# Kernel optimization log

Measured on AMD Instinct MI355X. Metric: run time of the kernel, lower is better.

## Reference

```python
import jax, jax.numpy as jnp
import numpy as np

B, T, H, W, D = 64, 512, 768, 256, 256  # batch, tokens, bert hidden, max words, embedding_dim


def setup_inputs() -> dict:
    key = jax.random.key(0)
    k1, k2, k3 = jax.random.split(key, 3)
    hidden_states = jax.random.normal(k1, (B, T, H), dtype=jnp.float32)
    # word_ids from a fast tokenizer are nondecreasing within a sentence
    word_ids = jnp.sort(jax.random.randint(k2, (B, T), 0, W), axis=-1)
    proj_w = jax.random.normal(k3, (H, D), dtype=jnp.float32) / np.sqrt(H).astype(np.float32)
    proj_b = jnp.zeros((D,), dtype=jnp.float32)
    return {"hidden_states": hidden_states, "word_ids": word_ids,
            "proj_w": proj_w, "proj_b": proj_b}


def _segment_mean(h, wid):
    # h: [T, H], wid: [T]. Invalid ids (<0 or >=W, i.e. special/pad tokens)
    # are routed to a dump segment W that is sliced away.
    idx = jnp.where((wid >= 0) & (wid < W), wid, W)
    sums = jax.ops.segment_sum(h, idx, num_segments=W + 1)[:W]          # [W, H]
    counts = jax.ops.segment_sum(jnp.ones((h.shape[0],), h.dtype), idx,
                                 num_segments=W + 1)[:W]                 # [W]
    # torch.clamp(counts, min=1) -> padded/empty words stay zero
    return sums / jnp.maximum(counts, 1.0)[:, None]


def reference(hidden_states, word_ids, proj_w, proj_b):
    # token-to-word scatter-mean pooling, vectorized over batch
    word_emb = jax.vmap(_segment_mean)(hidden_states, word_ids)  # [B, W, H]
    # final linear projection to embedding_dim
    return jnp.einsum('bwh,hd->bwd', word_emb, proj_w) + proj_b  # [B, W, D]
```

## Files before the change

kernel.cpp:

```cpp
#include <hip/hip_runtime.h>


#define NB 64
#define NT 512
#define NH 768
#define NW 256
#define ND 256
#define PAD 8
#define ROWE (NH + PAD)

typedef __attribute__((ext_vector_type(8))) short short8;
typedef __attribute__((ext_vector_type(4))) float f32x4;
typedef __attribute__((ext_vector_type(4))) float float4v;
typedef __attribute__((ext_vector_type(4))) unsigned short ushort4v;

__device__ __forceinline__ unsigned short f2bf(float f) {
    union { float f; unsigned u; } v; v.f = f;
    unsigned r = v.u + 0x7fffu + ((v.u >> 16) & 1u);
    return (unsigned short)(r >> 16);
}

__global__ void prep_wt2(const float* __restrict__ w, unsigned short* __restrict__ wt2) {
    __shared__ float tile[32][33];
    const int tid = threadIdx.x, n = blockIdx.x;
    const int tx = tid & 31, ty = tid >> 5;
    const int k0 = (n % 24) * 32, n0 = (n / 24) * 32;
    #pragma unroll
    for (int i = 0; i < 4; ++i)
        tile[ty + 8 * i][tx] = w[(size_t)(k0 + ty + 8 * i) * ND + n0 + tx];
    __syncthreads();
    if (tid < 128) {
        const int cc = tid & 31, q = tid >> 5;
        const int col = n0 + cc;
        ushort4v u0, u1;
        #pragma unroll
        for (int j = 0; j < 4; ++j) u0[j] = f2bf(tile[q * 8 + j][cc]);
        #pragma unroll
        for (int j = 0; j < 4; ++j) u1[j] = f2bf(tile[q * 8 + 4 + j][cc]);
        size_t off = (((size_t)(col >> 4) * 96 + (k0 >> 3) + q) * 16 + (col & 15)) * 8;
        *(ushort4v*)&wt2[off]     = u0;
        *(ushort4v*)&wt2[off + 4] = u1;
    }
}

__global__ __launch_bounds__(512, 4)
void fused(const float* __restrict__ hs, const int* __restrict__ wid,
           const unsigned short* __restrict__ wt2, const float* __restrict__ pb,
           float* __restrict__ out) {
    __shared__ unsigned short A[32][ROWE];
    __shared__ int swid[NT];
    __shared__ int sb[33];

    const int tid = threadIdx.x, bid = blockIdx.x;
    const int wave = tid >> 6, lane = tid & 63;
    const int b = bid >> 3, w0 = (bid & 7) * 32;

    swid[tid] = wid[b * NT + tid];
    __syncthreads();
    if (tid <= 32) {
        int v = w0 + tid, lo = 0, hi = NT;
        while (lo < hi) { int mid = (lo + hi) >> 1; if (swid[mid] < v) lo = mid + 1; else hi = mid; }
        sb[tid] = lo;
    }
    __syncthreads();

    const float* base = hs + (size_t)b * NT * NH + lane * 4;
    {
        const int s0 = sb[wave * 4],     s1 = sb[wave * 4 + 1];
        const int s2 = sb[wave * 4 + 2], s3 = sb[wave * 4 + 3];
        const int s4 = sb[wave * 4 + 4];

        float4v acc[4][3];
        #pragma unroll
        for (int r = 0; r < 4; ++r)
            #pragma unroll
            for (int c = 0; c < 3; ++c)
                #pragma unroll
                for (int q = 0; q < 4; ++q) acc[r][c][q] = 0.f;

#define ADD3(ar, vv) { _Pragma("unroll")                                      \
        for (int q = 0; q < 4; ++q) {                                         \
            ar[0][q] += (vv)[0][q]; ar[1][q] += (vv)[1][q]; ar[2][q] += (vv)[2][q]; } }
#define ROUTE4(tt, vv) {                                                      \
        if ((tt) < s1)      { ADD3(acc[0], vv); }                             \
        else if ((tt) < s2) { ADD3(acc[1], vv); }                             \
        else if ((tt) < s3) { ADD3(acc[2], vv); }                             \
        else                { ADD3(acc[3], vv); } }

        int t = s0;
        for (; t + 4 <= s4; t += 4) {
            float4v v[4][3];
            #pragma unroll
            for (int u = 0; u < 4; ++u) {
                const float* p2 = base + (size_t)(t + u) * NH;
                v[u][0] = *(const float4v*)(p2);
                v[u][1] = *(const float4v*)(p2 + 256);
                v[u][2] = *(const float4v*)(p2 + 512);
            }
            #pragma unroll
            for (int u = 0; u < 4; ++u) ROUTE4(t + u, v[u]);
        }
        for (; t < s4; ++t) {
            float4v v1[3];
            const float* p2 = base + (size_t)t * NH;
            v1[0] = *(const float4v*)(p2);
            v1[1] = *(const float4v*)(p2 + 256);
            v1[2] = *(const float4v*)(p2 + 512);
            ROUTE4(t, v1);
        }
#undef ROUTE4
#undef ADD3

        #pragma unroll
        for (int r = 0; r < 4; ++r) {
            const int row = wave * 4 + r;
            int cs = (r == 0) ? s0 : (r == 1) ? s1 : (r == 2) ? s2 : s3;
            int ce = (r == 0) ? s1 : (r == 1) ? s2 : (r == 2) ? s3 : s4;
            int cnt = ce - cs; if (cnt < 1) cnt = 1;
            const float sc = 1.0f / (float)cnt;
            #pragma unroll
            for (int c = 0; c < 3; ++c) {
                ushort4v u;
                #pragma unroll
                for (int q = 0; q < 4; ++q) u[q] = f2bf(acc[r][c][q] * sc);
                *(ushort4v*)&A[row][c * 256 + lane * 4] = u;
            }
        }
    }
    __syncthreads();

    const int cl = lane & 15, kg = lane >> 4;
    const int c0w = wave * 32;
    const unsigned short* bgp = wt2 + (size_t)(wave * 2) * 12288 + kg * 128 + cl * 8;

    short8 a0f[2], a1f[2], b0f[2], b1f[2];
    f32x4 acc[2][2];
    #pragma unroll
    for (int mt = 0; mt < 2; ++mt)
        #pragma unroll
        for (int nt = 0; nt < 2; ++nt)
            #pragma unroll
            for (int r = 0; r < 4; ++r) acc[mt][nt][r] = 0.f;

#define LDA(d, ks) { d[0] = *(const short8*)&A[cl][(ks) * 32 + kg * 8];       \
                     d[1] = *(const short8*)&A[16 + cl][(ks) * 32 + kg * 8]; }
#define LDB(d, ks) { _Pragma("unroll")                                        \
                     for (int nt = 0; nt < 2; ++nt)                           \
                         d[nt] = *(const short8*)(bgp + nt * 12288 + (ks) * 512); }
#define MM(a, bb) { _Pragma("unroll")                                         \
                    for (int mt = 0; mt < 2; ++mt)                            \
                        _Pragma("unroll")                                     \
                        for (int nt = 0; nt < 2; ++nt)                        \
                            acc[mt][nt] = __builtin_amdgcn_mfma_f32_16x16x32_bf16(a[mt], bb[nt], acc[mt][nt], 0, 0, 0); }

    LDA(a0f, 0); LDB(b0f, 0);
    #pragma unroll 1
    for (int i = 0; i < 12; ++i) {
        const int ks = 2 * i;
        LDA(a1f, ks + 1); LDB(b1f, ks + 1);
        MM(a0f, b0f);
        if (i < 11) { LDA(a0f, ks + 2); LDB(b0f, ks + 2); }
        MM(a1f, b1f);
    }
#undef LDA
#undef LDB
#undef MM

    float bv[2];
    bv[0] = pb[c0w + cl];
    bv[1] = pb[c0w + 16 + cl];

    #pragma unroll
    for (int mt = 0; mt < 2; ++mt)
        #pragma unroll
        for (int nt = 0; nt < 2; ++nt)
            #pragma unroll
            for (int r = 0; r < 4; ++r)
                out[((size_t)b * NW + w0 + mt * 16 + kg * 4 + r) * ND + c0w + nt * 16 + cl]
                    = acc[mt][nt][r] + bv[nt];
}

extern "C" void kernel_launch(void* const* d_in, const int* in_sizes, int n_in,
                              void* d_out, int out_size, void* d_ws, size_t ws_size,
                              hipStream_t stream) {
    const float* hs  = (const float*)d_in[0];
    const int*   wid = (const int*)d_in[1];
    const float* pw  = (const float*)d_in[2];
    const float* pb  = (const float*)d_in[3];
    float* out = (float*)d_out;

    unsigned short* wt2 = (unsigned short*)d_ws;

    prep_wt2<<<192, 256, 0, stream>>>(pw, wt2);
    fused<<<NB * (NW / 32), 512, 0, stream>>>(hs, wid, wt2, pb, out);
}
```

Measured before the change: 35.24 us.

## Balance segment-mean pooling across waves by token count instead of fixed word slots

Each wave no longer owns four fixed words. Work is now split by token count: each wave takes a contiguous run of whole words covering about one eighth of the block's tokens and keeps a single running accumulator that is flushed to LDS at each word boundary. The A tile is zero-filled up front so empty words still read as zero. This targets load imbalance when word lengths vary, and drops the four-way accumulator routing that cost registers. In exchange it adds data-dependent branches, a linear search for the start word, and an extra LDS zeroing pass.

```diff
diff --git a/kernel.cpp b/kernel.cpp
--- a/kernel.cpp
+++ b/kernel.cpp
@@ -12,6 +12,7 @@
 typedef __attribute__((ext_vector_type(8))) short short8;
 typedef __attribute__((ext_vector_type(4))) float f32x4;
 typedef __attribute__((ext_vector_type(4))) float float4v;
+typedef __attribute__((ext_vector_type(4))) unsigned int uint4v;
 typedef __attribute__((ext_vector_type(4))) unsigned short ushort4v;
 
 __device__ __forceinline__ unsigned short f2bf(float f) {
@@ -55,6 +56,16 @@
     const int wave = tid >> 6, lane = tid & 63;
     const int b = bid >> 3, w0 = (bid & 7) * 32;
 
+    {
+        uint4v z = {0, 0, 0, 0};
+        int c0 = tid * 6;
+        #pragma unroll
+        for (int i = 0; i < 6; ++i) {
+            int c = c0 + i;
+            int r = c / 96, k = (c % 96) * 8;
+            *(uint4v*)&A[r][k] = z;
+        }
+    }
     swid[tid] = wid[b * NT + tid];
     __syncthreads();
     if (tid <= 32) {
@@ -66,65 +77,68 @@
 
     const float* base = hs + (size_t)b * NT * NH + lane * 4;
     {
-        const int s0 = sb[wave * 4],     s1 = sb[wave * 4 + 1];
-        const int s2 = sb[wave * 4 + 2], s3 = sb[wave * 4 + 3];
-        const int s4 = sb[wave * 4 + 4];
-
-        float4v acc[4][3];
-        #pragma unroll
-        for (int r = 0; r < 4; ++r)
-            #pragma unroll
-            for (int c = 0; c < 3; ++c)
+        const int t0a = sb[0], total = sb[32] - sb[0];
+        int wa = 32, wb = 32;
+        {
+            const int tgA = t0a + (int)(((long)wave * total) >> 3);
+            const int tgB = t0a + (int)(((long)(wave + 1) * total) >> 3);
+            for (int i = 0; i <= 32; ++i) { if (sb[i] >= tgA) { wa = i; break; } }
+            for (int i = 0; i <= 32; ++i) { if (sb[i] >= tgB) { wb = i; break; } }
+        }
+        const int tstart = sb[wa], tend = sb[wb];
+
+        if (tstart < tend) {
+            int wptr = wa;
+            while (sb[wptr + 1] <= tstart) ++wptr;
+            int sEnd = sb[wptr + 1];
+            int segStart = tstart;
+
+            float4v ac0 = {0,0,0,0}, ac1 = {0,0,0,0}, ac2 = {0,0,0,0};
+
+#define FLUSH(t_) {                                                           \
+            const float sc_ = 1.0f / (float)(sEnd - segStart);                \
+            ushort4v uu_;                                                     \
+            _Pragma("unroll") for (int q_ = 0; q_ < 4; ++q_) uu_[q_] = f2bf(ac0[q_] * sc_); \
+            *(ushort4v*)&A[wptr][lane * 4] = uu_;                             \
+            _Pragma("unroll") for (int q_ = 0; q_ < 4; ++q_) uu_[q_] = f2bf(ac1[q_] * sc_); \
+            *(ushort4v*)&A[wptr][256 + lane * 4] = uu_;                       \
+            _Pragma("unroll") for (int q_ = 0; q_ < 4; ++q_) uu_[q_] = f2bf(ac2[q_] * sc_); \
+            *(ushort4v*)&A[wptr][512 + lane * 4] = uu_;                       \
+            ac0 = (float4v){0,0,0,0}; ac1 = (float4v){0,0,0,0}; ac2 = (float4v){0,0,0,0}; \
+            if ((t_) + 1 < tend) {                                            \
+                do { ++wptr; } while (sb[wptr + 1] <= (t_) + 1);              \
+                segStart = (t_) + 1; sEnd = sb[wptr + 1];                     \
+            }                                                                 \
+        }
+#define STEP(tt, v0, v1, v2) {                                                \
+            const int tcur_ = (tt);                                           \
+            _Pragma("unroll") for (int q_ = 0; q_ < 4; ++q_) {                \
+                ac0[q_] += (v0)[q_]; ac1[q_] += (v1)[q_]; ac2[q_] += (v2)[q_]; } \
+            if (tcur_ + 1 == sEnd) FLUSH(tcur_);                              \
+        }
+
+            int t = tstart;
+            for (; t + 4 <= tend; t += 4) {
+                float4v v[4][3];
                 #pragma unroll
-                for (int q = 0; q < 4; ++q) acc[r][c][q] = 0.f;
-
-#define ADD3(ar, vv) { _Pragma("unroll")                                      \
-        for (int q = 0; q < 4; ++q) {                                         \
-            ar[0][q] += (vv)[0][q]; ar[1][q] += (vv)[1][q]; ar[2][q] += (vv)[2][q]; } }
-#define ROUTE4(tt, vv) {                                                      \
-        if ((tt) < s1)      { ADD3(acc[0], vv); }                             \
-        else if ((tt) < s2) { ADD3(acc[1], vv); }                             \
-        else if ((tt) < s3) { ADD3(acc[2], vv); }                             \
-        else                { ADD3(acc[3], vv); } }
-
-        int t = s0;
-        for (; t + 4 <= s4; t += 4) {
-            float4v v[4][3];
-            #pragma unroll
-            for (int u = 0; u < 4; ++u) {
-                const float* p2 = base + (size_t)(t + u) * NH;
-                v[u][0] = *(const float4v*)(p2);
-                v[u][1] = *(const float4v*)(p2 + 256);
-                v[u][2] = *(const float4v*)(p2 + 512);
+                for (int u = 0; u < 4; ++u) {
+                    const float* p2 = base + (size_t)(t + u) * NH;
+                    v[u][0] = *(const float4v*)(p2);
+                    v[u][1] = *(const float4v*)(p2 + 256);
+                    v[u][2] = *(const float4v*)(p2 + 512);
+                }
+                #pragma unroll
+                for (int u = 0; u < 4; ++u) STEP(t + u, v[u][0], v[u][1], v[u][2]);
             }
-            #pragma unroll
-            for (int u = 0; u < 4; ++u) ROUTE4(t + u, v[u]);
-        }
-        for (; t < s4; ++t) {
-            float4v v1[3];
-            const float* p2 = base + (size_t)t * NH;
-            v1[0] = *(const float4v*)(p2);
-            v1[1] = *(const float4v*)(p2 + 256);
-            v1[2] = *(const float4v*)(p2 + 512);
-            ROUTE4(t, v1);
-        }
-#undef ROUTE4
-#undef ADD3
-
-        #pragma unroll
-        for (int r = 0; r < 4; ++r) {
-            const int row = wave * 4 + r;
-            int cs = (r == 0) ? s0 : (r == 1) ? s1 : (r == 2) ? s2 : s3;
-            int ce = (r == 0) ? s1 : (r == 1) ? s2 : (r == 2) ? s3 : s4;
-            int cnt = ce - cs; if (cnt < 1) cnt = 1;
-            const float sc = 1.0f / (float)cnt;
-            #pragma unroll
-            for (int c = 0; c < 3; ++c) {
-                ushort4v u;
-                #pragma unroll
-                for (int q = 0; q < 4; ++q) u[q] = f2bf(acc[r][c][q] * sc);
-                *(ushort4v*)&A[row][c * 256 + lane * 4] = u;
+            for (; t < tend; ++t) {
+                const float* p2 = base + (size_t)t * NH;
+                float4v v0 = *(const float4v*)(p2);
+                float4v v1 = *(const float4v*)(p2 + 256);
+                float4v v2 = *(const float4v*)(p2 + 512);
+                STEP(t, v0, v1, v2);
             }
+#undef STEP
+#undef FLUSH
         }
     }
     __syncthreads();
```

Result: no change. 35.82 us (+1.6%).

## Process two word tiles per block with warp-specialized pool/GEMM overlap

Applied to the files above, without the earlier changes.

Each block now handles 64 words instead of 32, with two LDS A-tiles. After all waves pool the first tile, four waves run the MFMA projection for it while the other four waves pool the second tile, and then all eight waves project the second tile. This aims to overlap the memory-bound pooling with the matrix-multiply phase and to halve the number of blocks. In exchange it doubles LDS use, lowers occupancy (launch bounds 4 down to 2), and splits the pooling work unevenly across waves.

```diff
diff --git a/kernel.cpp b/kernel.cpp
--- a/kernel.cpp
+++ b/kernel.cpp
@@ -43,141 +43,202 @@
     }
 }
 
-__global__ __launch_bounds__(512, 4)
+__device__ __forceinline__ void pool4(const int* __restrict__ sb, int wi,
+                                      unsigned short (*__restrict__ At)[ROWE], int rr,
+                                      const float* __restrict__ base, int lane) {
+    const int s0 = sb[wi],     s1 = sb[wi + 1];
+    const int s2 = sb[wi + 2], s3 = sb[wi + 3];
+    const int s4 = sb[wi + 4];
+
+    float4v acc[4][3];
+    #pragma unroll
+    for (int r = 0; r < 4; ++r)
+        #pragma unroll
+        for (int c = 0; c < 3; ++c)
+            #pragma unroll
+            for (int q = 0; q < 4; ++q) acc[r][c][q] = 0.f;
+
+#define ADD3_(ar, vv) { _Pragma("unroll")                                     \
+        for (int q = 0; q < 4; ++q) {                                         \
+            ar[0][q] += (vv)[0][q]; ar[1][q] += (vv)[1][q]; ar[2][q] += (vv)[2][q]; } }
+#define ROUTE4_(tt, vv) {                                                     \
+        if ((tt) < s1)      { ADD3_(acc[0], vv); }                            \
+        else if ((tt) < s2) { ADD3_(acc[1], vv); }                            \
+        else if ((tt) < s3) { ADD3_(acc[2], vv); }                            \
+        else                { ADD3_(acc[3], vv); } }
+
+    int t = s0;
+    for (; t + 4 <= s4; t += 4) {
+        float4v v[4][3];
+        #pragma unroll
+        for (int u = 0; u < 4; ++u) {
+            const float* p2 = base + (size_t)(t + u) * NH;
+            v[u][0] = *(const float4v*)(p2);
+            v[u][1] = *(const float4v*)(p2 + 256);
+            v[u][2] = *(const float4v*)(p2 + 512);
+        }
+        #pragma unroll
+        for (int u = 0; u < 4; ++u) ROUTE4_(t + u, v[u]);
+    }
+    for (; t < s4; ++t) {
+        float4v v1[3];
+        const float* p2 = base + (size_t)t * NH;
+        v1[0] = *(const float4v*)(p2);
+        v1[1] = *(const float4v*)(p2 + 256);
+        v1[2] = *(const float4v*)(p2 + 512);
+        ROUTE4_(t, v1);
+    }
+#undef ROUTE4_
+#undef ADD3_
+
+    #pragma unroll
+    for (int r = 0; r < 4; ++r) {
+        int cs = (r == 0) ? s0 : (r == 1) ? s1 : (r == 2) ? s2 : s3;
+        int ce = (r == 0) ? s1 : (r == 1) ? s2 : (r == 2) ? s3 : s4;
+        int cnt = ce - cs; if (cnt < 1) cnt = 1;
+        const float sc = 1.0f / (float)cnt;
+        #pragma unroll
+        for (int c = 0; c < 3; ++c) {
+            ushort4v u;
+            #pragma unroll
+            for (int q = 0; q < 4; ++q) u[q] = f2bf(acc[r][c][q] * sc);
+            *(ushort4v*)&At[rr + r][c * 256 + lane * 4] = u;
+        }
+    }
+}
+
+__global__ __launch_bounds__(512, 2)
 void fused(const float* __restrict__ hs, const int* __restrict__ wid,
            const unsigned short* __restrict__ wt2, const float* __restrict__ pb,
            float* __restrict__ out) {
-    __shared__ unsigned short A[32][ROWE];
+    __shared__ unsigned short A0t[32][ROWE];
+    __shared__ unsigned short A1t[32][ROWE];
     __shared__ int swid[NT];
-    __shared__ int sb[33];
+    __shared__ int sb[65];
 
     const int tid = threadIdx.x, bid = blockIdx.x;
     const int wave = tid >> 6, lane = tid & 63;
-    const int b = bid >> 3, w0 = (bid & 7) * 32;
+    const int b = bid >> 2, W0 = (bid & 3) * 64;
 
     swid[tid] = wid[b * NT + tid];
     __syncthreads();
-    if (tid <= 32) {
-        int v = w0 + tid, lo = 0, hi = NT;
+    if (tid <= 64) {
+        int v = W0 + tid, lo = 0, hi = NT;
         while (lo < hi) { int mid = (lo + hi) >> 1; if (swid[mid] < v) lo = mid + 1; else hi = mid; }
         sb[tid] = lo;
     }
     __syncthreads();
 
     const float* base = hs + (size_t)b * NT * NH + lane * 4;
+    const int cl = lane & 15, kg = lane >> 4;
+
+    pool4(sb, wave * 4, A0t, wave * 4, base, lane);
+    __syncthreads();
+
+    if (wave < 4) {
+        const int c0w = wave * 64;
+        const unsigned short* bgp = wt2 + (size_t)(wave * 4) * 12288 + kg * 128 + cl * 8;
+        short8 a0[2], a1[2], b0[4], b1[4];
+        f32x4 acc[2][4];
+        #pragma unroll
+        for (int mt = 0; mt < 2; ++mt)
+            #pragma unroll
+            for (int nt = 0; nt < 4; ++nt)
+                #pragma unroll
+                for (int r = 0; r < 4; ++r) acc[mt][nt][r] = 0.f;
+
+#define LDA0(d, ks) { d[0] = *(const short8*)&A0t[cl][(ks) * 32 + kg * 8];    \
+                      d[1] = *(const short8*)&A0t[16 + cl][(ks) * 32 + kg * 8]; }
+#define LDB0(d, ks) { _Pragma("unroll")                                       \
+                      for (int nt = 0; nt < 4; ++nt)                          \
+                          d[nt] = *(const short8*)(bgp + nt * 12288 + (ks) * 512); }
+#define MM0(a, bb) { _Pragma("unroll")                                        \
+                     for (int mt = 0; mt < 2; ++mt)                           \
+                         _Pragma("unroll")                                    \
+                         for (int nt = 0; nt < 4; ++nt)                       \
+                             acc[mt][nt] = __builtin_amdgcn_mfma_f32_16x16x32_bf16(a[mt], bb[nt], acc[mt][nt], 0, 0, 0); }
+
+        LDA0(a0, 0); LDB0(b0, 0);
+        #pragma unroll 1
+        for (int i = 0; i < 12; ++i) {
+            const int ks = 2 * i;
+            LDA0(a1, ks + 1); LDB0(b1, ks + 1);
+            MM0(a0, b0);
+            if (i < 11) { LDA0(a0, ks + 2); LDB0(b0, ks + 2); }
+            MM0(a1, b1);
+        }
+#undef LDA0
+#undef LDB0
+#undef MM0
+
+        float bv[4];
+        #pragma unroll
+        for (int nt = 0; nt < 4; ++nt) bv[nt] = pb[c0w + nt * 16 + cl];
+
+        #pragma unroll
+        for (int mt = 0; mt < 2; ++mt)
+            #pragma unroll
+            for (int nt = 0; nt < 4; ++nt)
+                #pragma unroll
+                for (int r = 0; r < 4; ++r)
+                    out[((size_t)b * NW + W0 + mt * 16 + kg * 4 + r) * ND + c0w + nt * 16 + cl]
+                        = acc[mt][nt][r] + bv[nt];
+    } else {
+        const int wv = wave - 4;
+        pool4(sb, 32 + wv * 8,     A1t, wv * 8,     base, lane);
+        pool4(sb, 32 + wv * 8 + 4, A1t, wv * 8 + 4, base, lane);
+    }
+    __syncthreads();
+
     {
-        const int s0 = sb[wave * 4],     s1 = sb[wave * 4 + 1];
-        const int s2 = sb[wave * 4 + 2], s3 = sb[wave * 4 + 3];
-        const int s4 = sb[wave * 4 + 4];
-
-        float4v acc[4][3];
-        #pragma unroll
-        for (int r = 0; r < 4; ++r)
-            #pragma unroll
-            for (int c = 0; c < 3; ++c)
-                #pragma unroll
-                for (int q = 0; q < 4; ++q) acc[r][c][q] = 0.f;
-
-#define ADD3(ar, vv) { _Pragma("unroll")                                      \
-        for (int q = 0; q < 4; ++q) {                                         \
-            ar[0][q] += (vv)[0][q]; ar[1][q] += (vv)[1][q]; ar[2][q] += (vv)[2][q]; } }
-#define ROUTE4(tt, vv) {                                                      \
-        if ((tt) < s1)      { ADD3(acc[0], vv); }                             \
-        else if ((tt) < s2) { ADD3(acc[1], vv); }                             \
-        else if ((tt) < s3) { ADD3(acc[2], vv); }                             \
-        else                { ADD3(acc[3], vv); } }
-
-        int t = s0;
-        for (; t + 4 <= s4; t += 4) {
-            float4v v[4][3];
-            #pragma unroll
-            for (int u = 0; u < 4; ++u) {
-                const float* p2 = base + (size_t)(t + u) * NH;
-                v[u][0] = *(const float4v*)(p2);
-                v[u][1] = *(const float4v*)(p2 + 256);
-                v[u][2] = *(const float4v*)(p2 + 512);
-            }
-            #pragma unroll
-            for (int u = 0; u < 4; ++u) ROUTE4(t + u, v[u]);
-        }
-        for (; t < s4; ++t) {
-            float4v v1[3];
-            const float* p2 = base + (size_t)t * NH;
-            v1[0] = *(const float4v*)(p2);
-            v1[1] = *(const float4v*)(p2 + 256);
-            v1[2] = *(const float4v*)(p2 + 512);
-            ROUTE4(t, v1);
-        }
-#undef ROUTE4
-#undef ADD3
-
-        #pragma unroll
-        for (int r = 0; r < 4; ++r) {
-            const int row = wave * 4 + r;
-            int cs = (r == 0) ? s0 : (r == 1) ? s1 : (r == 2) ? s2 : s3;
-            int ce = (r == 0) ? s1 : (r == 1) ? s2 : (r == 2) ? s3 : s4;
-            int cnt = ce - cs; if (cnt < 1) cnt = 1;
-            const float sc = 1.0f / (float)cnt;
-            #pragma unroll
-            for (int c = 0; c < 3; ++c) {
-                ushort4v u;
-                #pragma unroll
-                for (int q = 0; q < 4; ++q) u[q] = f2bf(acc[r][c][q] * sc);
-                *(ushort4v*)&A[row][c * 256 + lane * 4] = u;
-            }
-        }
-    }
-    __syncthreads();
-
-    const int cl = lane & 15, kg = lane >> 4;
-    const int c0w = wave * 32;
-    const unsigned short* bgp = wt2 + (size_t)(wave * 2) * 12288 + kg * 128 + cl * 8;
-
-    short8 a0f[2], a1f[2], b0f[2], b1f[2];
-    f32x4 acc[2][2];
-    #pragma unroll
-    for (int mt = 0; mt < 2; ++mt)
-        #pragma unroll
-        for (int nt = 0; nt < 2; ++nt)
-            #pragma unroll
-            for (int r = 0; r < 4; ++r) acc[mt][nt][r] = 0.f;
-
-#define LDA(d, ks) { d[0] = *(const short8*)&A[cl][(ks) * 32 + kg * 8];       \
-                     d[1] = *(const short8*)&A[16 + cl][(ks) * 32 + kg * 8]; }
-#define LDB(d, ks) { _Pragma("unroll")                                        \
-                     for (int nt = 0; nt < 2; ++nt)                           \
-                         d[nt] = *(const short8*)(bgp + nt * 12288 + (ks) * 512); }
-#define MM(a, bb) { _Pragma("unroll")                                         \
-                    for (int mt = 0; mt < 2; ++mt)                            \
-                        _Pragma("unroll")                                     \
-                        for (int nt = 0; nt < 2; ++nt)                        \
-                            acc[mt][nt] = __builtin_amdgcn_mfma_f32_16x16x32_bf16(a[mt], bb[nt], acc[mt][nt], 0, 0, 0); }
-
-    LDA(a0f, 0); LDB(b0f, 0);
-    #pragma unroll 1
-    for (int i = 0; i < 12; ++i) {
-        const int ks = 2 * i;
-        LDA(a1f, ks + 1); LDB(b1f, ks + 1);
-        MM(a0f, b0f);
-        if (i < 11) { LDA(a0f, ks + 2); LDB(b0f, ks + 2); }
-        MM(a1f, b1f);
-    }
-#undef LDA
-#undef LDB
-#undef MM
-
-    float bv[2];
-    bv[0] = pb[c0w + cl];
-    bv[1] = pb[c0w + 16 + cl];
-
-    #pragma unroll
-    for (int mt = 0; mt < 2; ++mt)
-        #pragma unroll
-        for (int nt = 0; nt < 2; ++nt)
-            #pragma unroll
-            for (int r = 0; r < 4; ++r)
-                out[((size_t)b * NW + w0 + mt * 16 + kg * 4 + r) * ND + c0w + nt * 16 + cl]
-                    = acc[mt][nt][r] + bv[nt];
+        const int c0w = wave * 32;
+        const unsigned short* bgp = wt2 + (size_t)(wave * 2) * 12288 + kg * 128 + cl * 8;
+        short8 a0f[2], a1f[2], b0f[2], b1f[2];
+        f32x4 acc[2][2];
+        #pragma unroll
+        for (int mt = 0; mt < 2; ++mt)
+            #pragma unroll
+            for (int nt = 0; nt < 2; ++nt)
+                #pragma unroll
+                for (int r = 0; r < 4; ++r) acc[mt][nt][r] = 0.f;
+
+#define LDA1(d, ks) { d[0] = *(const short8*)&A1t[cl][(ks) * 32 + kg * 8];    \
+                      d[1] = *(const short8*)&A1t[16 + cl][(ks) * 32 + kg * 8]; }
+#define LDB1(d, ks) { _Pragma("unroll")                                       \
+                      for (int nt = 0; nt < 2; ++nt)                          \
+                          d[nt] = *(const short8*)(bgp + nt * 12288 + (ks) * 512); }
+#define MM1(a, bb) { _Pragma("unroll")                                        \
+                     for (int mt = 0; mt < 2; ++mt)                           \
+                         _Pragma("unroll")                                    \
+                         for (int nt = 0; nt < 2; ++nt)                       \
+                             acc[mt][nt] = __builtin_amdgcn_mfma_f32_16x16x32_bf16(a[mt], bb[nt], acc[mt][nt], 0, 0, 0); }
+
+        LDA1(a0f, 0); LDB1(b0f, 0);
+        #pragma unroll 1
+        for (int i = 0; i < 12; ++i) {
+            const int ks = 2 * i;
+            LDA1(a1f, ks + 1); LDB1(b1f, ks + 1);
+            MM1(a0f, b0f);
+            if (i < 11) { LDA1(a0f, ks + 2); LDB1(b0f, ks + 2); }
+            MM1(a1f, b1f);
+        }
+#undef LDA1
+#undef LDB1
+#undef MM1
+
+        float bv[2];
+        bv[0] = pb[c0w + cl];
+        bv[1] = pb[c0w + 16 + cl];
+
+        #pragma unroll
+        for (int mt = 0; mt < 2; ++mt)
+            #pragma unroll
+            for (int nt = 0; nt < 2; ++nt)
+                #pragma unroll
+                for (int r = 0; r < 4; ++r)
+                    out[((size_t)b * NW + W0 + 32 + mt * 16 + kg * 4 + r) * ND + c0w + nt * 16 + cl]
+                        = acc[mt][nt][r] + bv[nt];
+    }
 }
 
 extern "C" void kernel_launch(void* const* d_in, const int* in_sizes, int n_in,
@@ -192,5 +253,5 @@
     unsigned short* wt2 = (unsigned short*)d_ws;
 
     prep_wt2<<<192, 256, 0, stream>>>(pw, wt2);
-    fused<<<NB * (NW / 32), 512, 0, stream>>>(hs, wid, wt2, pb, out);
-}
+    fused<<<NB * 4, 512, 0, stream>>>(hs, wid, wt2, pb, out);
+}
```

Result: faster. 34.42 us (median of 4 runs) (-2.3%).
